# Optimization experiments

Hardware: AMD Instinct MI355X
Metric: run time of the kernel (lower is better)

The kernel has to match this reference:

```python
import jax, jax.numpy as jnp
import numpy as np

N = 100000   # nodes
E = 1600000  # edges
D = 128      # feature dim (layers all 128)
G = 512      # graphs in batch
C = 10       # num_classes
EPS = 1e-5   # batchnorm eps


def setup_inputs() -> dict:
    key = jax.random.key(0)
    ks = jax.random.split(key, 16)
    s = 1.0 / np.sqrt(D)
    return {
        "x": jax.random.normal(ks[0], (N, D), jnp.float32),
        "edge_index": jax.random.randint(ks[1], (2, E), 0, N),
        "batch": jnp.sort(jax.random.randint(ks[2], (N,), 0, G)),
        "w1": jax.random.normal(ks[3], (D, D), jnp.float32) * s,
        "b1": jnp.zeros((D,), jnp.float32),
        "w2": jax.random.normal(ks[4], (D, D), jnp.float32) * s,
        "b2": jnp.zeros((D,), jnp.float32),
        "w3": jax.random.normal(ks[5], (D, D), jnp.float32) * s,
        "b3": jnp.zeros((D,), jnp.float32),
        "g1": jnp.ones((D,), jnp.float32),
        "be1": jnp.zeros((D,), jnp.float32),
        "g2": jnp.ones((D,), jnp.float32),
        "be2": jnp.zeros((D,), jnp.float32),
        "fc_w": jax.random.normal(ks[6], (D, C), jnp.float32) * s,
        "fc_b": jnp.zeros((C,), jnp.float32),
    }


def _gcn(x, src, dst, norm, W, b):
    # transform -> gather -> normalize -> scatter-add (PyG GCNConv)
    h = x @ W
    out = jax.ops.segment_sum(h[src] * norm[:, None], dst, num_segments=x.shape[0])
    return out + b


def _bn(x, g, b):
    # training-mode BatchNorm1d: batch mean / biased variance
    mu = jnp.mean(x, axis=0)
    var = jnp.mean((x - mu) ** 2, axis=0)
    return (x - mu) * jax.lax.rsqrt(var + EPS) * g + b


def reference(x, edge_index, batch, w1, b1, w2, b2, w3, b3, g1, be1, g2, be2, fc_w, fc_b):
    n = x.shape[0]
    loop = jnp.arange(n)
    src = jnp.concatenate([edge_index[0], loop])  # add self-loops
    dst = jnp.concatenate([edge_index[1], loop])
    deg = jax.ops.segment_sum(jnp.ones_like(src, x.dtype), dst, num_segments=n)
    dinv = jax.lax.rsqrt(jnp.maximum(deg, 1.0))  # deg >= 1 due to self-loops
    norm = dinv[src] * dinv[dst]  # symmetric normalization per edge

    h = jax.nn.relu(_gcn(x, src, dst, norm, w1, b1))        # conv1 + relu (bn1 unused, per source)
    h = jax.nn.relu(_gcn(h, src, dst, norm, w2, b2))        # conv2 + relu
    h = jax.nn.relu(_bn(h, g1, be1))                        # bn + relu
    h = jax.nn.relu(_gcn(h, src, dst, norm, w3, b3))        # conv3 + relu
    h = jax.nn.relu(_bn(h, g2, be2))                        # bn + relu

    cnt = jax.ops.segment_sum(jnp.ones((n,), h.dtype), batch, num_segments=G)
    pooled = jax.ops.segment_sum(h, batch, num_segments=G) / jnp.maximum(cnt, 1.0)[:, None]
    logits = pooled @ fc_w + fc_b
    return jax.nn.log_softmax(logits, axis=1)
```

## Files before the change

kernel.cpp:

```cpp
#include <hip/hip_runtime.h>
#include <hip/hip_bf16.h>
#include <math.h>

#define D 128
#define G_GRAPHS 512
#define C_CLASSES 10
#define BN_EPS 1e-5f
#define NBUCK_MAX 512
#define EDGE_CHUNK 4096
#define EPT 16

typedef unsigned short u16;
typedef unsigned int u32;
typedef unsigned short ushort4_t __attribute__((ext_vector_type(4)));
typedef unsigned short ushort8_t __attribute__((ext_vector_type(8)));
typedef __bf16 bf16x8 __attribute__((ext_vector_type(8)));
typedef float floatx4 __attribute__((ext_vector_type(4)));
union B8 { ushort8_t u; bf16x8 b; };

__device__ __forceinline__ float bf_lo(u32 v) { return __uint_as_float(v << 16); }
__device__ __forceinline__ float bf_hi(u32 v) { return __uint_as_float(v & 0xffff0000u); }
__device__ __forceinline__ u16 f2bf(float f) {
    union { float f; u32 u; } x; x.f = f;
    u32 r = x.u + 0x7fff + ((x.u >> 16) & 1);
    return (u16)(r >> 16);
}
__device__ __forceinline__ u32 pack2bf(float a, float b) {
    return (u32)f2bf(a) | ((u32)f2bf(b) << 16);
}


__global__ __launch_bounds__(256) void bucket_hist_kernel(
    const int* __restrict__ dst, int* __restrict__ bucketCnt, int E, int nbuck)
{
    __shared__ int h[NBUCK_MAX];
    int tid = threadIdx.x;
    for (int i = tid; i < NBUCK_MAX; i += 256) h[i] = 0;
    __syncthreads();
    for (int i = blockIdx.x * 256 + tid; i < E; i += gridDim.x * 256)
        atomicAdd(&h[dst[i] >> 8], 1);
    __syncthreads();
    for (int i = tid; i < nbuck; i += 256)
        if (h[i]) atomicAdd(&bucketCnt[i], h[i]);
}

__global__ void scan_buckets_kernel(
    const int* __restrict__ bucketCnt, int* __restrict__ bucketBase,
    int* __restrict__ bucketCursor, int* __restrict__ rowPtr, int nbuck, int N, int E)
{
    __shared__ int buf[2][512];
    int tid = threadIdx.x;
    int v = (tid < nbuck) ? bucketCnt[tid] : 0;
    buf[0][tid] = v;
    __syncthreads();
    int cur = 0;
    for (int off = 1; off < 512; off <<= 1) {
        buf[1 - cur][tid] = buf[cur][tid] + ((tid >= off) ? buf[cur][tid - off] : 0);
        cur ^= 1;
        __syncthreads();
    }
    if (tid < nbuck) {
        int b = buf[cur][tid] - v;
        bucketBase[tid] = b;
        bucketCursor[tid] = b;
    }
    if (tid == 0) { bucketBase[nbuck] = E; rowPtr[N] = E; }
}

__global__ __launch_bounds__(256) void scatter_pairs_kernel(
    const int* __restrict__ src, const int* __restrict__ dst,
    int* __restrict__ bucketCursor, u32* __restrict__ pairs, int E)
{
    __shared__ int h[NBUCK_MAX];
    __shared__ int base[NBUCK_MAX];
    int tid = threadIdx.x;
    int e0 = blockIdx.x * EDGE_CHUNK;
    for (int i = tid; i < NBUCK_MAX; i += 256) h[i] = 0;
    __syncthreads();
    int s[EPT], d[EPT], r[EPT];
#pragma unroll
    for (int j = 0; j < EPT; ++j) {
        int i = e0 + j * 256 + tid;
        if (i < E) {
            s[j] = src[i];
            d[j] = dst[i];
            r[j] = atomicAdd(&h[d[j] >> 8], 1);
        } else {
            d[j] = -1;
        }
    }
    __syncthreads();
    for (int i = tid; i < NBUCK_MAX; i += 256)
        if (h[i]) base[i] = atomicAdd(&bucketCursor[i], h[i]);
    __syncthreads();
#pragma unroll
    for (int j = 0; j < EPT; ++j) {
        if (d[j] >= 0) {
            int b = d[j] >> 8;
            pairs[base[b] + r[j]] = ((u32)s[j] << 8) | (u32)(d[j] & 255);
        }
    }
}

__global__ __launch_bounds__(256) void bucket_sort_kernel(
    const u32* __restrict__ pairs, const int* __restrict__ bucketBase,
    int* __restrict__ colIdx, int* __restrict__ rowPtr, float* __restrict__ dinv, int N)
{
    __shared__ int h[256];
    __shared__ int cur[256];
    __shared__ int sbuf[2][256];
    int tid = threadIdx.x;
    int b = blockIdx.x;
    int s = bucketBase[b], e = bucketBase[b + 1];
    h[tid] = 0;
    __syncthreads();
    for (int i = s + tid; i < e; i += 256)
        atomicAdd(&h[pairs[i] & 255], 1);
    __syncthreads();
    int cnt = h[tid];
    sbuf[0][tid] = cnt;
    __syncthreads();
    int c = 0;
    for (int off = 1; off < 256; off <<= 1) {
        sbuf[1 - c][tid] = sbuf[c][tid] + ((tid >= off) ? sbuf[c][tid - off] : 0);
        c ^= 1;
        __syncthreads();
    }
    int excl = sbuf[c][tid] - cnt;
    int v = b * 256 + tid;
    if (v < N) {
        rowPtr[v] = s + excl;
        dinv[v] = rsqrtf((float)(cnt + 1));
    }
    cur[tid] = s + excl;
    __syncthreads();
    for (int i = s + tid; i < e; i += 256) {
        u32 p = pairs[i];
        int pos = atomicAdd(&cur[p & 255], 1);
        colIdx[pos] = (int)(p >> 8);
    }
}

__global__ __launch_bounds__(256) void graph_bounds_kernel(
    const int* __restrict__ batch, int* __restrict__ gstart, int N)
{
    int i = blockIdx.x * 256 + threadIdx.x;
    if (i >= N) return;
    int b = batch[i];
    int prev = (i == 0) ? -1 : batch[i - 1];
    if (b != prev) {
        for (int g = prev + 1; g <= b; ++g) gstart[g] = i;
    }
    if (i == N - 1) {
        for (int g = b + 1; g <= G_GRAPHS; ++g) gstart[g] = N;
    }
}

__global__ __launch_bounds__(256) void wconv_kernel(
    const float4* __restrict__ w1, const float4* __restrict__ w2,
    const float4* __restrict__ w3, u16* __restrict__ wtAll)
{
    const float4* W = (blockIdx.x == 0) ? w1 : (blockIdx.x == 1) ? w2 : w3;
    u16* Wt = wtAll + (size_t)blockIdx.x * D * D;
    int tid = threadIdx.x;
#pragma unroll
    for (int i = 0; i < 16; ++i) {
        int idx = tid + i * 256;
        int k = idx >> 5, c4 = idx & 31;
        float4 v = W[idx];
        Wt[(4 * c4 + 0) * D + k] = f2bf(v.x);
        Wt[(4 * c4 + 1) * D + k] = f2bf(v.y);
        Wt[(4 * c4 + 2) * D + k] = f2bf(v.z);
        Wt[(4 * c4 + 3) * D + k] = f2bf(v.w);
    }
}

#define XS_STRIDE 136

__device__ __forceinline__ void gemm_core_and_store(
    const u16* Xs, const u16* Ws, u16* __restrict__ Y, int row0, int nrows, int tid)
{
    int wid = tid >> 6, lane = tid & 63;
    int m = lane & 15, quad = lane >> 4;
    int xrow = wid * 16 + m;

    floatx4 acc[8] = {};
#pragma unroll
    for (int ks = 0; ks < 4; ++ks) {
        int kk = ks * 32 + quad * 8;
        B8 a;
        a.u = *(const ushort8_t*)&Xs[xrow * XS_STRIDE + kk];
#pragma unroll
        for (int t = 0; t < 8; ++t) {
            B8 b;
            b.u = *(const ushort8_t*)&Ws[(t * 16 + m) * XS_STRIDE + kk];
            acc[t] = __builtin_amdgcn_mfma_f32_16x16x32_bf16(b.b, a.b, acc[t], 0, 0, 0);
        }
    }
    int grow = row0 + xrow;
    if (grow < nrows) {
#pragma unroll
        for (int t = 0; t < 8; ++t) {
            ushort4_t o;
            o.x = f2bf(acc[t][0]); o.y = f2bf(acc[t][1]);
            o.z = f2bf(acc[t][2]); o.w = f2bf(acc[t][3]);
            *(ushort4_t*)&Y[(size_t)grow * D + t * 16 + quad * 4] = o;
        }
    }
}

__device__ __forceinline__ void stage_w(const u16* __restrict__ Wt, u16* Ws, int tid) {
    const ushort8_t* Wv = (const ushort8_t*)Wt;
#pragma unroll
    for (int i = 0; i < 8; ++i) {
        int idx = tid + i * 256;
        int n = idx >> 4, c8 = idx & 15;
        *(ushort8_t*)&Ws[n * XS_STRIDE + c8 * 8] = Wv[idx];
    }
}

__global__ __launch_bounds__(256) void gemm_mfma_f32in_kernel(
    const float4* __restrict__ X, const u16* __restrict__ Wt,
    u16* __restrict__ Y, int nrows)
{
    __shared__ __align__(16) u16 Xs[64 * XS_STRIDE];
    __shared__ __align__(16) u16 Ws[128 * XS_STRIDE];
    int tid = threadIdx.x;
    int row0 = blockIdx.x * 64;
    stage_w(Wt, Ws, tid);
#pragma unroll
    for (int i = 0; i < 8; ++i) {
        int idx = tid + i * 256;
        int r = idx >> 5, c4 = idx & 31;
        int gr = row0 + r;
        float4 v = make_float4(0.f, 0.f, 0.f, 0.f);
        if (gr < nrows) v = X[(size_t)gr * 32 + c4];
        ushort4_t o;
        o.x = f2bf(v.x); o.y = f2bf(v.y); o.z = f2bf(v.z); o.w = f2bf(v.w);
        *(ushort4_t*)&Xs[r * XS_STRIDE + c4 * 4] = o;
    }
    __syncthreads();
    gemm_core_and_store(Xs, Ws, Y, row0, nrows, tid);
}

__global__ __launch_bounds__(256) void gemm_mfma_bf16in_kernel(
    const uint4* __restrict__ X, const u16* __restrict__ Wt,
    const float* __restrict__ scale, const float* __restrict__ shift,
    u16* __restrict__ Y, int nrows)
{
    __shared__ __align__(16) u16 Xs[64 * XS_STRIDE];
    __shared__ __align__(16) u16 Ws[128 * XS_STRIDE];
    int tid = threadIdx.x;
    int row0 = blockIdx.x * 64;
    bool fuse = (scale != nullptr);
    stage_w(Wt, Ws, tid);
#pragma unroll
    for (int i = 0; i < 4; ++i) {
        int idx = tid + i * 256;
        int r = idx >> 4, c8 = idx & 15;
        int gr = row0 + r;
        uint4 v = make_uint4(0, 0, 0, 0);
        if (gr < nrows) v = X[(size_t)gr * 16 + c8];
        if (fuse) {
            int k = c8 * 8;
            v.x = pack2bf(fmaxf(bf_lo(v.x) * scale[k]     + shift[k],     0.f),
                          fmaxf(bf_hi(v.x) * scale[k + 1] + shift[k + 1], 0.f));
            v.y = pack2bf(fmaxf(bf_lo(v.y) * scale[k + 2] + shift[k + 2], 0.f),
                          fmaxf(bf_hi(v.y) * scale[k + 3] + shift[k + 3], 0.f));
            v.z = pack2bf(fmaxf(bf_lo(v.z) * scale[k + 4] + shift[k + 4], 0.f),
                          fmaxf(bf_hi(v.z) * scale[k + 5] + shift[k + 5], 0.f));
            v.w = pack2bf(fmaxf(bf_lo(v.w) * scale[k + 6] + shift[k + 6], 0.f),
                          fmaxf(bf_hi(v.w) * scale[k + 7] + shift[k + 7], 0.f));
        }
        *(uint4*)&Xs[r * XS_STRIDE + c8 * 8] = v;
    }
    __syncthreads();
    gemm_core_and_store(Xs, Ws, Y, row0, nrows, tid);
}

#define ACC8(tw, duu)                                              \
    acc[0] += (duu) * bf_lo((tw).x); acc[1] += (duu) * bf_hi((tw).x); \
    acc[2] += (duu) * bf_lo((tw).y); acc[3] += (duu) * bf_hi((tw).y); \
    acc[4] += (duu) * bf_lo((tw).z); acc[5] += (duu) * bf_hi((tw).z); \
    acc[6] += (duu) * bf_lo((tw).w); acc[7] += (duu) * bf_hi((tw).w);

__global__ __launch_bounds__(256) void aggregate_kernel(
    const uint4* __restrict__ T, const int* __restrict__ colIdx,
    const int* __restrict__ rowPtr, const float* __restrict__ dinv,
    const float* __restrict__ bias, u32* __restrict__ outH, int n)
{
    int wid = threadIdx.x >> 6;
    int lane = threadIdx.x & 63;
    int row = blockIdx.x * 4 + wid;
    if (row >= n) return;
    int fg = lane & 15;
    int eg = lane >> 4;

    float dr = dinv[row];
    float acc[8] = {};

    if (eg == 0) {
        uint4 sv = T[(size_t)row * 16 + fg];
        acc[0] = dr * bf_lo(sv.x); acc[1] = dr * bf_hi(sv.x);
        acc[2] = dr * bf_lo(sv.y); acc[3] = dr * bf_hi(sv.y);
        acc[4] = dr * bf_lo(sv.z); acc[5] = dr * bf_hi(sv.z);
        acc[6] = dr * bf_lo(sv.w); acc[7] = dr * bf_hi(sv.w);
    }

    int s = rowPtr[row], e = rowPtr[row + 1];
    for (int j0 = s; j0 < e; j0 += 64) {
        int m = e - j0;
        if (m > 64) m = 64;
        int u = row;
        float du = 0.f;
        if (lane < m) {
            u = colIdx[j0 + lane];
            du = dinv[u];
        }
        int nc = (m + 15) >> 4;
        for (int c = 0; c < nc; ++c) {
            int b0 = c * 16 + eg;
            int u0 = __shfl(u, b0);      int u1 = __shfl(u, b0 + 4);
            int u2 = __shfl(u, b0 + 8);  int u3 = __shfl(u, b0 + 12);
            float d0 = __shfl(du, b0);      float d1 = __shfl(du, b0 + 4);
            float d2 = __shfl(du, b0 + 8);  float d3 = __shfl(du, b0 + 12);
            uint4 t0 = T[(size_t)u0 * 16 + fg];
            uint4 t1 = T[(size_t)u1 * 16 + fg];
            uint4 t2 = T[(size_t)u2 * 16 + fg];
            uint4 t3 = T[(size_t)u3 * 16 + fg];
            ACC8(t0, d0); ACC8(t1, d1); ACC8(t2, d2); ACC8(t3, d3);
        }
    }

#pragma unroll
    for (int off = 16; off < 64; off <<= 1) {
#pragma unroll
        for (int i = 0; i < 8; ++i) acc[i] += __shfl_xor(acc[i], off);
    }

    const float2* bp = (const float2*)bias;
    int pidx = fg * 4 + eg;
    float2 b = bp[pidx];
    float ox = fmaxf(dr * acc[eg * 2] + b.x, 0.f);
    float oy = fmaxf(dr * acc[eg * 2 + 1] + b.y, 0.f);
    outH[(size_t)row * 64 + pidx] = pack2bf(ox, oy);
}

__global__ __launch_bounds__(256) void bn_stats_kernel(
    const u32* __restrict__ H, int n, float* __restrict__ gsum, float* __restrict__ gsq)
{
    int tid = threadIdx.x;
    int c = tid & 63, rr = tid >> 6;
    float sA = 0.f, sA2 = 0.f, sB = 0.f, sB2 = 0.f;
    for (int row = blockIdx.x * 4 + rr; row < n; row += gridDim.x * 4) {
        u32 v = H[(size_t)row * 64 + c];
        float a = bf_lo(v), b = bf_hi(v);
        sA += a; sA2 += a * a; sB += b; sB2 += b * b;
    }
    __shared__ float shA[256], shA2[256], shB[256], shB2[256];
    shA[tid] = sA; shA2[tid] = sA2; shB[tid] = sB; shB2[tid] = sB2;
    __syncthreads();
    if (tid < 64) {
        float tA = shA[tid] + shA[tid + 64] + shA[tid + 128] + shA[tid + 192];
        float tA2 = shA2[tid] + shA2[tid + 64] + shA2[tid + 128] + shA2[tid + 192];
        float tB = shB[tid] + shB[tid + 64] + shB[tid + 128] + shB[tid + 192];
        float tB2 = shB2[tid] + shB2[tid + 64] + shB2[tid + 128] + shB2[tid + 192];
        atomicAdd(&gsum[2 * c], tA);
        atomicAdd(&gsq[2 * c], tA2);
        atomicAdd(&gsum[2 * c + 1], tB);
        atomicAdd(&gsq[2 * c + 1], tB2);
    }
}

__global__ void bn_finalize_kernel(const float* __restrict__ gsum, const float* __restrict__ gsq,
                                   const float* __restrict__ gamma, const float* __restrict__ beta,
                                   float n, float* __restrict__ scale, float* __restrict__ shift)
{
    int c = threadIdx.x;
    float mu = gsum[c] / n;
    float var = gsq[c] / n - mu * mu;
    float sc = gamma[c] * rsqrtf(var + BN_EPS);
    scale[c] = sc;
    shift[c] = beta[c] - mu * sc;
}

__global__ __launch_bounds__(256) void pool_kernel(
    const u32* __restrict__ H, const float* __restrict__ scale, const float* __restrict__ shift,
    const int* __restrict__ gstart, float* __restrict__ pooled)
{
    int g = blockIdx.x;
    int tid = threadIdx.x;
    int c = tid & 63, q = tid >> 6;
    int s = gstart[g], cnt = gstart[g + 1] - s;
    float scA = scale[2 * c], shA = shift[2 * c];
    float scB = scale[2 * c + 1], shB = shift[2 * c + 1];
    float aA = 0.f, aB = 0.f;
    for (int i = q; i < cnt; i += 4) {
        u32 v = H[(size_t)(s + i) * 64 + c];
        aA += fmaxf(bf_lo(v) * scA + shA, 0.f);
        aB += fmaxf(bf_hi(v) * scB + shB, 0.f);
    }
    __shared__ float shAa[256], shBb[256];
    shAa[tid] = aA; shBb[tid] = aB;
    __syncthreads();
    if (tid < 64) {
        float tA = shAa[tid] + shAa[tid + 64] + shAa[tid + 128] + shAa[tid + 192];
        float tB = shBb[tid] + shBb[tid + 64] + shBb[tid + 128] + shBb[tid + 192];
        float inv = 1.f / (float)(cnt > 1 ? cnt : 1);
        ((float2*)pooled)[(size_t)g * 64 + c] = make_float2(tA * inv, tB * inv);
    }
}

__global__ __launch_bounds__(64) void classify_kernel(
    const float* __restrict__ pooled, const float* __restrict__ fcw,
    const float* __restrict__ fcb, float* __restrict__ out)
{
    int g = blockIdx.x;
    int tid = threadIdx.x;
    __shared__ float prow[D];
    __shared__ float lg[C_CLASSES];
    prow[tid] = pooled[(size_t)g * D + tid];
    prow[tid + 64] = pooled[(size_t)g * D + 64 + tid];
    __syncthreads();
    if (tid < C_CLASSES) {
        float s = fcb[tid];
        for (int d = 0; d < D; ++d) s += prow[d] * fcw[d * C_CLASSES + tid];
        lg[tid] = s;
    }
    __syncthreads();
    if (tid == 0) {
        float m = -1e30f;
        for (int c = 0; c < C_CLASSES; ++c) m = fmaxf(m, lg[c]);
        float se = 0.f;
        for (int c = 0; c < C_CLASSES; ++c) se += expf(lg[c] - m);
        float lse = m + logf(se);
        for (int c = 0; c < C_CLASSES; ++c) out[(size_t)g * C_CLASSES + c] = lg[c] - lse;
    }
}

extern "C" void kernel_launch(void* const* d_in, const int* in_sizes, int n_in,
                              void* d_out, int out_size, void* d_ws, size_t ws_size,
                              hipStream_t stream) {
    const float* x   = (const float*)d_in[0];
    const int* ei    = (const int*)d_in[1];
    const int* batch = (const int*)d_in[2];
    const float* w1  = (const float*)d_in[3];
    const float* b1  = (const float*)d_in[4];
    const float* w2  = (const float*)d_in[5];
    const float* b2  = (const float*)d_in[6];
    const float* w3  = (const float*)d_in[7];
    const float* b3  = (const float*)d_in[8];
    const float* g1  = (const float*)d_in[9];
    const float* be1 = (const float*)d_in[10];
    const float* g2  = (const float*)d_in[11];
    const float* be2 = (const float*)d_in[12];
    const float* fcw = (const float*)d_in[13];
    const float* fcb = (const float*)d_in[14];

    const int N = in_sizes[0] / D;
    const int E = in_sizes[1] / 2;
    const int* src = ei;
    const int* dst = ei + E;
    const int nbuck = (N + 255) >> 8;

    char* p = (char*)d_ws;
    auto alloc = [&](size_t bytes) -> void* {
        void* r = (void*)p;
        p += (bytes + 255) & ~(size_t)255;
        return r;
    };
    float* dinv     = (float*)alloc((size_t)N * 4);
    int*   rowPtr   = (int*)alloc((size_t)(N + 1) * 4);
    int*   colIdx   = (int*)alloc((size_t)E * 4);
    u32*   pairs    = (u32*)alloc((size_t)E * 4);
    int*   bucketCnt    = (int*)alloc(NBUCK_MAX * 4);
    int*   bucketBase   = (int*)alloc((NBUCK_MAX + 1) * 4);
    int*   bucketCursor = (int*)alloc(NBUCK_MAX * 4);
    int*   gstart  = (int*)alloc((G_GRAPHS + 1) * 4);
    float* statsacc= (float*)alloc(4 * D * 4);
    float* gsum1 = statsacc, *gsq1 = statsacc + D, *gsum2 = statsacc + 2 * D, *gsq2 = statsacc + 3 * D;
    float* sc1     = (float*)alloc(D * 4);
    float* sh1     = (float*)alloc(D * 4);
    float* sc2     = (float*)alloc(D * 4);
    float* sh2     = (float*)alloc(D * 4);
    float* pooled  = (float*)alloc((size_t)G_GRAPHS * D * 4);
    u16*   wtAll   = (u16*)alloc((size_t)3 * D * D * 2);
    u16*   tmp     = (u16*)alloc((size_t)N * D * 2);
    u16*   hbuf    = (u16*)alloc((size_t)N * D * 2);

    hipMemsetAsync(bucketCnt, 0, NBUCK_MAX * 4, stream);
    hipMemsetAsync(statsacc, 0, 4 * D * 4, stream);

    bucket_hist_kernel<<<512, 256, 0, stream>>>(dst, bucketCnt, E, nbuck);
    scan_buckets_kernel<<<1, 512, 0, stream>>>(bucketCnt, bucketBase, bucketCursor, rowPtr, nbuck, N, E);
    scatter_pairs_kernel<<<(E + EDGE_CHUNK - 1) / EDGE_CHUNK, 256, 0, stream>>>(src, dst, bucketCursor, pairs, E);
    bucket_sort_kernel<<<nbuck, 256, 0, stream>>>(pairs, bucketBase, colIdx, rowPtr, dinv, N);
    graph_bounds_kernel<<<(N + 255) / 256, 256, 0, stream>>>(batch, gstart, N);
    wconv_kernel<<<3, 256, 0, stream>>>((const float4*)w1, (const float4*)w2, (const float4*)w3, wtAll);

    const int GB = (N + 63) / 64;
    const int AB = (N + 3) / 4;

    gemm_mfma_f32in_kernel<<<GB, 256, 0, stream>>>((const float4*)x, wtAll, tmp, N);
    aggregate_kernel<<<AB, 256, 0, stream>>>((const uint4*)tmp, colIdx, rowPtr, dinv, b1, (u32*)hbuf, N);
    gemm_mfma_bf16in_kernel<<<GB, 256, 0, stream>>>((const uint4*)hbuf, wtAll + D * D, nullptr, nullptr, tmp, N);
    aggregate_kernel<<<AB, 256, 0, stream>>>((const uint4*)tmp, colIdx, rowPtr, dinv, b2, (u32*)hbuf, N);
    bn_stats_kernel<<<256, 256, 0, stream>>>((const u32*)hbuf, N, gsum1, gsq1);
    bn_finalize_kernel<<<1, 128, 0, stream>>>(gsum1, gsq1, g1, be1, (float)N, sc1, sh1);
    gemm_mfma_bf16in_kernel<<<GB, 256, 0, stream>>>((const uint4*)hbuf, wtAll + 2 * D * D, sc1, sh1, tmp, N);
    aggregate_kernel<<<AB, 256, 0, stream>>>((const uint4*)tmp, colIdx, rowPtr, dinv, b3, (u32*)hbuf, N);
    bn_stats_kernel<<<256, 256, 0, stream>>>((const u32*)hbuf, N, gsum2, gsq2);
    bn_finalize_kernel<<<1, 128, 0, stream>>>(gsum2, gsq2, g2, be2, (float)N, sc2, sh2);
    pool_kernel<<<G_GRAPHS, 256, 0, stream>>>((const u32*)hbuf, sc2, sh2, gstart, pooled);
    classify_kernel<<<G_GRAPHS, 64, 0, stream>>>(pooled, fcw, fcb, (float*)d_out);
}
```

Measured before the change: 520.7 us.

## Persistent GEMM grid, fold BN finalize into consumers, fuse pool+classify, merge memsets

```diff
diff --git a/kernel.cpp b/kernel.cpp
--- a/kernel.cpp
+++ b/kernel.cpp
@@ -176,6 +176,7 @@
 }
 
 #define XS_STRIDE 136
+#define GEMM_GRID 768
 
 __device__ __forceinline__ void gemm_core_and_store(
     const u16* Xs, const u16* Ws, u16* __restrict__ Y, int row0, int nrows, int tid)
@@ -221,61 +222,76 @@
 
 __global__ __launch_bounds__(256) void gemm_mfma_f32in_kernel(
     const float4* __restrict__ X, const u16* __restrict__ Wt,
-    u16* __restrict__ Y, int nrows)
+    u16* __restrict__ Y, int nrows, int ntiles)
 {
     __shared__ __align__(16) u16 Xs[64 * XS_STRIDE];
     __shared__ __align__(16) u16 Ws[128 * XS_STRIDE];
     int tid = threadIdx.x;
-    int row0 = blockIdx.x * 64;
     stage_w(Wt, Ws, tid);
-#pragma unroll
-    for (int i = 0; i < 8; ++i) {
-        int idx = tid + i * 256;
-        int r = idx >> 5, c4 = idx & 31;
-        int gr = row0 + r;
-        float4 v = make_float4(0.f, 0.f, 0.f, 0.f);
-        if (gr < nrows) v = X[(size_t)gr * 32 + c4];
-        ushort4_t o;
-        o.x = f2bf(v.x); o.y = f2bf(v.y); o.z = f2bf(v.z); o.w = f2bf(v.w);
-        *(ushort4_t*)&Xs[r * XS_STRIDE + c4 * 4] = o;
-    }
-    __syncthreads();
-    gemm_core_and_store(Xs, Ws, Y, row0, nrows, tid);
+    for (int t = blockIdx.x; t < ntiles; t += gridDim.x) {
+        int row0 = t * 64;
+        __syncthreads();
+#pragma unroll
+        for (int i = 0; i < 8; ++i) {
+            int idx = tid + i * 256;
+            int r = idx >> 5, c4 = idx & 31;
+            int gr = row0 + r;
+            float4 v = make_float4(0.f, 0.f, 0.f, 0.f);
+            if (gr < nrows) v = X[(size_t)gr * 32 + c4];
+            ushort4_t o;
+            o.x = f2bf(v.x); o.y = f2bf(v.y); o.z = f2bf(v.z); o.w = f2bf(v.w);
+            *(ushort4_t*)&Xs[r * XS_STRIDE + c4 * 4] = o;
+        }
+        __syncthreads();
+        gemm_core_and_store(Xs, Ws, Y, row0, nrows, tid);
+    }
 }
 
 __global__ __launch_bounds__(256) void gemm_mfma_bf16in_kernel(
     const uint4* __restrict__ X, const u16* __restrict__ Wt,
-    const float* __restrict__ scale, const float* __restrict__ shift,
-    u16* __restrict__ Y, int nrows)
+    const float* __restrict__ gsum, const float* __restrict__ gsq,
+    const float* __restrict__ gamma, const float* __restrict__ beta, float invN,
+    u16* __restrict__ Y, int nrows, int ntiles)
 {
     __shared__ __align__(16) u16 Xs[64 * XS_STRIDE];
     __shared__ __align__(16) u16 Ws[128 * XS_STRIDE];
-    int tid = threadIdx.x;
-    int row0 = blockIdx.x * 64;
-    bool fuse = (scale != nullptr);
+    __shared__ float scs[D], shs[D];
+    int tid = threadIdx.x;
+    bool fuse = (gsum != nullptr);
     stage_w(Wt, Ws, tid);
-#pragma unroll
-    for (int i = 0; i < 4; ++i) {
-        int idx = tid + i * 256;
-        int r = idx >> 4, c8 = idx & 15;
-        int gr = row0 + r;
-        uint4 v = make_uint4(0, 0, 0, 0);
-        if (gr < nrows) v = X[(size_t)gr * 16 + c8];
-        if (fuse) {
-            int k = c8 * 8;
-            v.x = pack2bf(fmaxf(bf_lo(v.x) * scale[k]     + shift[k],     0.f),
-                          fmaxf(bf_hi(v.x) * scale[k + 1] + shift[k + 1], 0.f));
-            v.y = pack2bf(fmaxf(bf_lo(v.y) * scale[k + 2] + shift[k + 2], 0.f),
-                          fmaxf(bf_hi(v.y) * scale[k + 3] + shift[k + 3], 0.f));
-            v.z = pack2bf(fmaxf(bf_lo(v.z) * scale[k + 4] + shift[k + 4], 0.f),
-                          fmaxf(bf_hi(v.z) * scale[k + 5] + shift[k + 5], 0.f));
-            v.w = pack2bf(fmaxf(bf_lo(v.w) * scale[k + 6] + shift[k + 6], 0.f),
-                          fmaxf(bf_hi(v.w) * scale[k + 7] + shift[k + 7], 0.f));
-        }
-        *(uint4*)&Xs[r * XS_STRIDE + c8 * 8] = v;
-    }
-    __syncthreads();
-    gemm_core_and_store(Xs, Ws, Y, row0, nrows, tid);
+    if (fuse && tid < D) {
+        float mu = gsum[tid] * invN;
+        float var = gsq[tid] * invN - mu * mu;
+        float sc = gamma[tid] * rsqrtf(var + BN_EPS);
+        scs[tid] = sc;
+        shs[tid] = beta[tid] - mu * sc;
+    }
+    for (int t = blockIdx.x; t < ntiles; t += gridDim.x) {
+        int row0 = t * 64;
+        __syncthreads();
+#pragma unroll
+        for (int i = 0; i < 4; ++i) {
+            int idx = tid + i * 256;
+            int r = idx >> 4, c8 = idx & 15;
+            int gr = row0 + r;
+            uint4 v = make_uint4(0, 0, 0, 0);
+            if (gr < nrows) v = X[(size_t)gr * 16 + c8];
+            if (fuse) {
+                int k = c8 * 8;
+                v.x = pack2bf(fmaxf(bf_lo(v.x) * scs[k]     + shs[k],     0.f),
+                              fmaxf(bf_hi(v.x) * scs[k + 1] + shs[k + 1], 0.f));
+                v.y = pack2bf(fmaxf(bf_lo(v.y) * scs[k + 2] + shs[k + 2], 0.f),
+                              fmaxf(bf_hi(v.y) * scs[k + 3] + shs[k + 3], 0.f));
+                v.z = pack2bf(fmaxf(bf_lo(v.z) * scs[k + 4] + shs[k + 4], 0.f),
+                              fmaxf(bf_hi(v.z) * scs[k + 5] + shs[k + 5], 0.f));
+                v.w = pack2bf(fmaxf(bf_lo(v.w) * scs[k + 6] + shs[k + 6], 0.f),
+                              fmaxf(bf_hi(v.w) * scs[k + 7] + shs[k + 7], 0.f));
+            }
+            *(uint4*)&Xs[r * XS_STRIDE + c8 * 8] = v;
+        }
+        __syncthreads();
+        gemm_core_and_store(Xs, Ws, Y, row0, nrows, tid);
+    }
 }
 
 #define ACC8(tw, duu)                                              \
@@ -295,6 +311,7 @@
     if (row >= n) return;
     int fg = lane & 15;
     int eg = lane >> 4;
+    const char* baseT = (const char*)T + fg * 16;
 
     float dr = dinv[row];
     float acc[8] = {};
@@ -311,23 +328,24 @@
     for (int j0 = s; j0 < e; j0 += 64) {
         int m = e - j0;
         if (m > 64) m = 64;
-        int u = row;
+        u32 voff = (u32)row << 8;
         float du = 0.f;
         if (lane < m) {
-            u = colIdx[j0 + lane];
+            int u = colIdx[j0 + lane];
+            voff = (u32)u << 8;
             du = dinv[u];
         }
         int nc = (m + 15) >> 4;
         for (int c = 0; c < nc; ++c) {
             int b0 = c * 16 + eg;
-            int u0 = __shfl(u, b0);      int u1 = __shfl(u, b0 + 4);
-            int u2 = __shfl(u, b0 + 8);  int u3 = __shfl(u, b0 + 12);
+            u32 o0 = (u32)__shfl((int)voff, b0);      u32 o1 = (u32)__shfl((int)voff, b0 + 4);
+            u32 o2 = (u32)__shfl((int)voff, b0 + 8);  u32 o3 = (u32)__shfl((int)voff, b0 + 12);
             float d0 = __shfl(du, b0);      float d1 = __shfl(du, b0 + 4);
             float d2 = __shfl(du, b0 + 8);  float d3 = __shfl(du, b0 + 12);
-            uint4 t0 = T[(size_t)u0 * 16 + fg];
-            uint4 t1 = T[(size_t)u1 * 16 + fg];
-            uint4 t2 = T[(size_t)u2 * 16 + fg];
-            uint4 t3 = T[(size_t)u3 * 16 + fg];
+            uint4 t0 = *(const uint4*)(baseT + o0);
+            uint4 t1 = *(const uint4*)(baseT + o1);
+            uint4 t2 = *(const uint4*)(baseT + o2);
+            uint4 t3 = *(const uint4*)(baseT + o3);
             ACC8(t0, d0); ACC8(t1, d1); ACC8(t2, d2); ACC8(t3, d3);
         }
     }
@@ -372,69 +390,53 @@
     }
 }
 
-__global__ void bn_finalize_kernel(const float* __restrict__ gsum, const float* __restrict__ gsq,
-                                   const float* __restrict__ gamma, const float* __restrict__ beta,
-                                   float n, float* __restrict__ scale, float* __restrict__ shift)
-{
-    int c = threadIdx.x;
-    float mu = gsum[c] / n;
-    float var = gsq[c] / n - mu * mu;
-    float sc = gamma[c] * rsqrtf(var + BN_EPS);
-    scale[c] = sc;
-    shift[c] = beta[c] - mu * sc;
-}
-
-__global__ __launch_bounds__(256) void pool_kernel(
-    const u32* __restrict__ H, const float* __restrict__ scale, const float* __restrict__ shift,
-    const int* __restrict__ gstart, float* __restrict__ pooled)
+__global__ __launch_bounds__(256) void pool_classify_kernel(
+    const u32* __restrict__ H, const float* __restrict__ gsum, const float* __restrict__ gsq,
+    const float* __restrict__ gamma, const float* __restrict__ beta, float invN,
+    const int* __restrict__ gstart, const float* __restrict__ fcw,
+    const float* __restrict__ fcb, float* __restrict__ out)
 {
     int g = blockIdx.x;
     int tid = threadIdx.x;
     int c = tid & 63, q = tid >> 6;
+    float muA = gsum[2 * c] * invN, muB = gsum[2 * c + 1] * invN;
+    float vA = gsq[2 * c] * invN - muA * muA, vB = gsq[2 * c + 1] * invN - muB * muB;
+    float scA = gamma[2 * c] * rsqrtf(vA + BN_EPS), scB = gamma[2 * c + 1] * rsqrtf(vB + BN_EPS);
+    float shA = beta[2 * c] - muA * scA, shB = beta[2 * c + 1] - muB * scB;
+
     int s = gstart[g], cnt = gstart[g + 1] - s;
-    float scA = scale[2 * c], shA = shift[2 * c];
-    float scB = scale[2 * c + 1], shB = shift[2 * c + 1];
     float aA = 0.f, aB = 0.f;
     for (int i = q; i < cnt; i += 4) {
         u32 v = H[(size_t)(s + i) * 64 + c];
         aA += fmaxf(bf_lo(v) * scA + shA, 0.f);
         aB += fmaxf(bf_hi(v) * scB + shB, 0.f);
     }
-    __shared__ float shAa[256], shBb[256];
-    shAa[tid] = aA; shBb[tid] = aB;
-    __syncthreads();
-    if (tid < 64) {
-        float tA = shAa[tid] + shAa[tid + 64] + shAa[tid + 128] + shAa[tid + 192];
-        float tB = shBb[tid] + shBb[tid + 64] + shBb[tid + 128] + shBb[tid + 192];
-        float inv = 1.f / (float)(cnt > 1 ? cnt : 1);
-        ((float2*)pooled)[(size_t)g * 64 + c] = make_float2(tA * inv, tB * inv);
-    }
-}
-
-__global__ __launch_bounds__(64) void classify_kernel(
-    const float* __restrict__ pooled, const float* __restrict__ fcw,
-    const float* __restrict__ fcb, float* __restrict__ out)
-{
-    int g = blockIdx.x;
-    int tid = threadIdx.x;
+    __shared__ float sA[256], sB[256];
     __shared__ float prow[D];
     __shared__ float lg[C_CLASSES];
-    prow[tid] = pooled[(size_t)g * D + tid];
-    prow[tid + 64] = pooled[(size_t)g * D + 64 + tid];
+    sA[tid] = aA; sB[tid] = aB;
+    __syncthreads();
+    if (tid < 64) {
+        float tA = sA[tid] + sA[tid + 64] + sA[tid + 128] + sA[tid + 192];
+        float tB = sB[tid] + sB[tid + 64] + sB[tid + 128] + sB[tid + 192];
+        float inv = 1.f / (float)(cnt > 1 ? cnt : 1);
+        prow[2 * tid] = tA * inv;
+        prow[2 * tid + 1] = tB * inv;
+    }
     __syncthreads();
     if (tid < C_CLASSES) {
-        float s = fcb[tid];
-        for (int d = 0; d < D; ++d) s += prow[d] * fcw[d * C_CLASSES + tid];
-        lg[tid] = s;
+        float sum = fcb[tid];
+        for (int d = 0; d < D; ++d) sum += prow[d] * fcw[d * C_CLASSES + tid];
+        lg[tid] = sum;
     }
     __syncthreads();
     if (tid == 0) {
-        float m = -1e30f;
-        for (int c = 0; c < C_CLASSES; ++c) m = fmaxf(m, lg[c]);
+        float mx = -1e30f;
+        for (int k = 0; k < C_CLASSES; ++k) mx = fmaxf(mx, lg[k]);
         float se = 0.f;
-        for (int c = 0; c < C_CLASSES; ++c) se += expf(lg[c] - m);
-        float lse = m + logf(se);
-        for (int c = 0; c < C_CLASSES; ++c) out[(size_t)g * C_CLASSES + c] = lg[c] - lse;
+        for (int k = 0; k < C_CLASSES; ++k) se += expf(lg[k] - mx);
+        float lse = mx + logf(se);
+        for (int k = 0; k < C_CLASSES; ++k) out[(size_t)g * C_CLASSES + k] = lg[k] - lse;
     }
 }
 
@@ -462,6 +464,7 @@
     const int* src = ei;
     const int* dst = ei + E;
     const int nbuck = (N + 255) >> 8;
+    const float invN = 1.f / (float)N;
 
     char* p = (char*)d_ws;
     auto alloc = [&](size_t bytes) -> void* {
@@ -469,27 +472,21 @@
         p += (bytes + 255) & ~(size_t)255;
         return r;
     };
+    int*   bucketCnt    = (int*)alloc(NBUCK_MAX * 4);
+    float* statsacc     = (float*)alloc(4 * D * 4);
+    float* gsum1 = statsacc, *gsq1 = statsacc + D, *gsum2 = statsacc + 2 * D, *gsq2 = statsacc + 3 * D;
     float* dinv     = (float*)alloc((size_t)N * 4);
     int*   rowPtr   = (int*)alloc((size_t)(N + 1) * 4);
     int*   colIdx   = (int*)alloc((size_t)E * 4);
     u32*   pairs    = (u32*)alloc((size_t)E * 4);
-    int*   bucketCnt    = (int*)alloc(NBUCK_MAX * 4);
     int*   bucketBase   = (int*)alloc((NBUCK_MAX + 1) * 4);
     int*   bucketCursor = (int*)alloc(NBUCK_MAX * 4);
     int*   gstart  = (int*)alloc((G_GRAPHS + 1) * 4);
-    float* statsacc= (float*)alloc(4 * D * 4);
-    float* gsum1 = statsacc, *gsq1 = statsacc + D, *gsum2 = statsacc + 2 * D, *gsq2 = statsacc + 3 * D;
-    float* sc1     = (float*)alloc(D * 4);
-    float* sh1     = (float*)alloc(D * 4);
-    float* sc2     = (float*)alloc(D * 4);
-    float* sh2     = (float*)alloc(D * 4);
-    float* pooled  = (float*)alloc((size_t)G_GRAPHS * D * 4);
     u16*   wtAll   = (u16*)alloc((size_t)3 * D * D * 2);
     u16*   tmp     = (u16*)alloc((size_t)N * D * 2);
     u16*   hbuf    = (u16*)alloc((size_t)N * D * 2);
 
-    hipMemsetAsync(bucketCnt, 0, NBUCK_MAX * 4, stream);
-    hipMemsetAsync(statsacc, 0, 4 * D * 4, stream);
+    hipMemsetAsync(bucketCnt, 0, NBUCK_MAX * 4 + 4 * D * 4, stream);
 
     bucket_hist_kernel<<<512, 256, 0, stream>>>(dst, bucketCnt, E, nbuck);
     scan_buckets_kernel<<<1, 512, 0, stream>>>(bucketCnt, bucketBase, bucketCursor, rowPtr, nbuck, N, E);
@@ -498,19 +495,20 @@
     graph_bounds_kernel<<<(N + 255) / 256, 256, 0, stream>>>(batch, gstart, N);
     wconv_kernel<<<3, 256, 0, stream>>>((const float4*)w1, (const float4*)w2, (const float4*)w3, wtAll);
 
-    const int GB = (N + 63) / 64;
+    const int NT = (N + 63) / 64;
+    const int GB = NT < GEMM_GRID ? NT : GEMM_GRID;
     const int AB = (N + 3) / 4;
 
-    gemm_mfma_f32in_kernel<<<GB, 256, 0, stream>>>((const float4*)x, wtAll, tmp, N);
+    gemm_mfma_f32in_kernel<<<GB, 256, 0, stream>>>((const float4*)x, wtAll, tmp, N, NT);
     aggregate_kernel<<<AB, 256, 0, stream>>>((const uint4*)tmp, colIdx, rowPtr, dinv, b1, (u32*)hbuf, N);
-    gemm_mfma_bf16in_kernel<<<GB, 256, 0, stream>>>((const uint4*)hbuf, wtAll + D * D, nullptr, nullptr, tmp, N);
+    gemm_mfma_bf16in_kernel<<<GB, 256, 0, stream>>>((const uint4*)hbuf, wtAll + D * D,
+        nullptr, nullptr, nullptr, nullptr, 0.f, tmp, N, NT);
     aggregate_kernel<<<AB, 256, 0, stream>>>((const uint4*)tmp, colIdx, rowPtr, dinv, b2, (u32*)hbuf, N);
     bn_stats_kernel<<<256, 256, 0, stream>>>((const u32*)hbuf, N, gsum1, gsq1);
-    bn_finalize_kernel<<<1, 128, 0, stream>>>(gsum1, gsq1, g1, be1, (float)N, sc1, sh1);
-    gemm_mfma_bf16in_kernel<<<GB, 256, 0, stream>>>((const uint4*)hbuf, wtAll + 2 * D * D, sc1, sh1, tmp, N);
+    gemm_mfma_bf16in_kernel<<<GB, 256, 0, stream>>>((const uint4*)hbuf, wtAll + 2 * D * D,
+        gsum1, gsq1, g1, be1, invN, tmp, N, NT);
     aggregate_kernel<<<AB, 256, 0, stream>>>((const uint4*)tmp, colIdx, rowPtr, dinv, b3, (u32*)hbuf, N);
     bn_stats_kernel<<<256, 256, 0, stream>>>((const u32*)hbuf, N, gsum2, gsq2);
-    bn_finalize_kernel<<<1, 128, 0, stream>>>(gsum2, gsq2, g2, be2, (float)N, sc2, sh2);
-    pool_kernel<<<G_GRAPHS, 256, 0, stream>>>((const u32*)hbuf, sc2, sh2, gstart, pooled);
-    classify_kernel<<<G_GRAPHS, 64, 0, stream>>>(pooled, fcw, fcb, (float*)d_out);
-}
+    pool_classify_kernel<<<G_GRAPHS, 256, 0, stream>>>((const u32*)hbuf, gsum2, gsq2, g2, be2, invN,
+        gstart, fcw, fcb, (float*)d_out);
+}
```

New measurement: 510.2 us. 2.0% less time.
